# Performance work log

Measured on AMD Instinct MI355X. Metric: run time of the kernel, lower is better.

Reference implementation:

```python
import jax, jax.numpy as jnp
import numpy as np

N_NODES = 50000
N_EDGES = 800000
IN_CH = 128
HID = 64
OUT_CH = 64


def sage_conv(x, src, dst, w_l, w_r, b, num_nodes):
    """PyG SAGEConv with mean aggregation: lin_l(mean_j x_j) + lin_r(x_i)."""
    # gather source features and scatter-mean into destination nodes
    agg = jax.ops.segment_sum(x[src], dst, num_segments=num_nodes)          # [N, C]
    deg = jax.ops.segment_sum(jnp.ones((src.shape[0],), x.dtype), dst,
                              num_segments=num_nodes)                        # [N]
    mean = agg / jnp.maximum(deg, 1.0)[:, None]
    return mean @ w_l + x @ w_r + b


def setup_inputs() -> dict:
    key = jax.random.key(0)
    k = jax.random.split(key, 8)
    x = jax.random.normal(k[0], (N_NODES, IN_CH), dtype=jnp.float32)
    edge_index = jax.random.randint(k[1], (2, N_EDGES), 0, N_NODES, dtype=jnp.int32)
    s1 = 1.0 / np.sqrt(IN_CH)
    s2 = 1.0 / np.sqrt(HID)
    w1_l = jax.random.uniform(k[2], (IN_CH, HID), jnp.float32, -s1, s1)
    w1_r = jax.random.uniform(k[3], (IN_CH, HID), jnp.float32, -s1, s1)
    b1 = jax.random.uniform(k[4], (HID,), jnp.float32, -s1, s1)
    w2_l = jax.random.uniform(k[5], (HID, OUT_CH), jnp.float32, -s2, s2)
    w2_r = jax.random.uniform(k[6], (HID, OUT_CH), jnp.float32, -s2, s2)
    b2 = jax.random.uniform(k[7], (OUT_CH,), jnp.float32, -s2, s2)
    return {"x": x, "edge_index": edge_index,
            "w1_l": w1_l, "w1_r": w1_r, "b1": b1,
            "w2_l": w2_l, "w2_r": w2_r, "b2": b2}


def reference(x, edge_index, w1_l, w1_r, b1, w2_l, w2_r, b2):
    src, dst = edge_index[0], edge_index[1]
    num_nodes = x.shape[0]
    h = jax.nn.relu(sage_conv(x, src, dst, w1_l, w1_r, b1, num_nodes))
    out = jax.nn.relu(sage_conv(h, src, dst, w2_l, w2_r, b2, num_nodes))
    return out
```

## Files before the change

kernel.cpp:

```cpp
#include <hip/hip_runtime.h>
#include <hip/hip_fp16.h>

#define DEGCAP 64
#define NB_MAX 256
#define BCAP 5120
#define TILE 4000

typedef _Float16 half8 __attribute__((ext_vector_type(8)));
typedef float float4v __attribute__((ext_vector_type(4)));

__global__ __launch_bounds__(256) void prep(int* __restrict__ bCursor,
                                            const float* __restrict__ w1l,
                                            const float* __restrict__ w1r,
                                            const float* __restrict__ w2l,
                                            const float* __restrict__ w2r,
                                            _Float16* __restrict__ Wt1,
                                            _Float16* __restrict__ Wt2) {
    const int gtid = blockIdx.x * 256 + threadIdx.x;
    const int gstride = gridDim.x * 256;
    if (gtid < NB_MAX) bCursor[gtid] = 0;
    for (int i = gtid; i < 128 * 128; i += gstride) {
        int c = i >> 7, k = i & 127;
        const float* W = (c < 64) ? w1l : w1r;
        Wt1[c * 128 + k] = (_Float16)W[k * 64 + (c & 63)];
    }
    for (int i = gtid; i < 128 * 64; i += gstride) {
        int c = i >> 6, k = i & 63;
        const float* W = (c < 64) ? w2l : w2r;
        Wt2[c * 64 + k] = (_Float16)W[k * 64 + (c & 63)];
    }
}

template <int K, bool AF32>
__device__ __forceinline__ void gemm_body(const void* __restrict__ Av,
                                          const _Float16* __restrict__ Wt,
                                          unsigned short* __restrict__ Clh,
                                          unsigned short* __restrict__ Trh,
                                          int M, int blk) {
    constexpr int NS = K / 32;
    const int tid = threadIdx.x;
    const int row0 = blk * 64;
    const int wv = tid >> 6;
    const int lane = tid & 63;
    const int qd = lane >> 4;
    const int lr = lane & 15;
    const int col = wv * 16 + lr;

    half8 bl[NS], br[NS];
    #pragma unroll
    for (int s = 0; s < NS; ++s) {
        bl[s] = *(const half8*)&Wt[col * K + s * 32 + qd * 8];
        br[s] = *(const half8*)&Wt[(64 + col) * K + s * 32 + qd * 8];
    }

    half8 a[4][NS];
    #pragma unroll
    for (int i = 0; i < 4; ++i) {
        const int gr = row0 + i * 16 + lr;
        const bool ok = gr < M;
        if constexpr (AF32) {
            const float* Arow = (const float*)Av + (long long)gr * K;
            #pragma unroll
            for (int s = 0; s < NS; ++s) {
                float4 t0 = make_float4(0.f, 0.f, 0.f, 0.f);
                float4 t1 = make_float4(0.f, 0.f, 0.f, 0.f);
                if (ok) {
                    t0 = *(const float4*)&Arow[s * 32 + qd * 8];
                    t1 = *(const float4*)&Arow[s * 32 + qd * 8 + 4];
                }
                half8 h;
                h[0] = (_Float16)t0.x; h[1] = (_Float16)t0.y;
                h[2] = (_Float16)t0.z; h[3] = (_Float16)t0.w;
                h[4] = (_Float16)t1.x; h[5] = (_Float16)t1.y;
                h[6] = (_Float16)t1.z; h[7] = (_Float16)t1.w;
                a[i][s] = h;
            }
        } else {
            const _Float16* Arow = (const _Float16*)Av + (long long)gr * K;
            #pragma unroll
            for (int s = 0; s < NS; ++s) {
                a[i][s] = ok ? *(const half8*)&Arow[s * 32 + qd * 8]
                             : (half8){0, 0, 0, 0, 0, 0, 0, 0};
            }
        }
    }

    float4v accL[4], accR[4];
    #pragma unroll
    for (int i = 0; i < 4; ++i) {
        accL[i] = (float4v){0.f, 0.f, 0.f, 0.f};
        accR[i] = (float4v){0.f, 0.f, 0.f, 0.f};
    }

    #pragma unroll
    for (int i = 0; i < 4; ++i) {
        #pragma unroll
        for (int s = 0; s < NS; ++s) {
            accL[i] = __builtin_amdgcn_mfma_f32_16x16x32_f16(a[i][s], bl[s], accL[i], 0, 0, 0);
            accR[i] = __builtin_amdgcn_mfma_f32_16x16x32_f16(a[i][s], br[s], accR[i], 0, 0, 0);
        }
    }

    #pragma unroll
    for (int i = 0; i < 4; ++i) {
        #pragma unroll
        for (int rg = 0; rg < 4; ++rg) {
            int gr = row0 + i * 16 + qd * 4 + rg;
            if (gr < M) {
                Clh[(long long)gr * 64 + col] = __half_as_ushort(__float2half_rn(accL[i][rg]));
                Trh[(long long)gr * 64 + col] = __half_as_ushort(__float2half_rn(accR[i][rg]));
            }
        }
    }
}

__global__ __launch_bounds__(256) void fused_scatter_gemm1(
        const int* __restrict__ src, const int* __restrict__ dst,
        int* __restrict__ bCursor, unsigned int* __restrict__ gPacked,
        int E, int NB, int scatterBlocks,
        const float* __restrict__ A, const _Float16* __restrict__ Wt1,
        unsigned short* __restrict__ Clh, unsigned short* __restrict__ Trh,
        int M) {
    __shared__ __align__(16) char smem[22048];
    const int tid = threadIdx.x;

    if ((int)blockIdx.x < scatterBlocks) {
        unsigned int* spv = (unsigned int*)smem;
        unsigned char* sbuk = (unsigned char*)(smem + 16000);
        int* hist = (int*)(smem + 20000);
        int* cur  = (int*)(smem + 21024);

        const int t0 = blockIdx.x * TILE;
        const int len = (E - t0) < TILE ? (E - t0) : TILE;

        hist[tid] = 0;
        __syncthreads();
        for (int j = tid; j < len; j += 256) {
            int d = dst[t0 + j];
            int s = src[t0 + j];
            int b = d >> 8;
            sbuk[j] = (unsigned char)b;
            spv[j] = ((unsigned int)(d & 255) << 17) | (unsigned int)s;
            atomicAdd(&hist[b], 1);
        }
        __syncthreads();
        if (tid < NB && hist[tid] > 0)
            cur[tid] = tid * BCAP + atomicAdd(&bCursor[tid], hist[tid]);
        __syncthreads();
        for (int j = tid; j < len; j += 256) {
            int b = sbuk[j];
            int pos = atomicAdd(&cur[b], 1);
            if (pos < (b + 1) * BCAP) gPacked[pos] = spv[j];
        }
    } else {
        gemm_body<128, true>(A, Wt1, Clh, Trh, M, (int)blockIdx.x - scatterBlocks);
    }
}

__global__ __launch_bounds__(256) void bucket_build(const unsigned int* __restrict__ gPacked,
                                                    const int* __restrict__ bCursor,
                                                    int* __restrict__ deg,
                                                    unsigned short* __restrict__ ssrc,
                                                    int N) {
    __shared__ int cnt[256];
    const int tid = threadIdx.x;
    const int b = blockIdx.x;
    const int base = b * BCAP;
    int C = bCursor[b];
    if (C > BCAP) C = BCAP;

    cnt[tid] = 0;
    __syncthreads();
    for (int j = tid; j < C; j += 256) {
        unsigned int v = gPacked[base + j];
        int ln = v >> 17;
        int pos = atomicAdd(&cnt[ln], 1);
        if (pos < DEGCAP)
            ssrc[(long long)(b * 256 + ln) * DEGCAP + pos] = (unsigned short)(v & 0x1FFFFu);
    }
    __syncthreads();
    int node = b * 256 + tid;
    if (node < N) deg[node] = cnt[tid] < DEGCAP ? cnt[tid] : DEGCAP;
}

__global__ __launch_bounds__(256) void gemm2(const _Float16* __restrict__ Ah,
                                             const _Float16* __restrict__ Wt2,
                                             unsigned short* __restrict__ Clh,
                                             unsigned short* __restrict__ Trh,
                                             int M) {
    gemm_body<64, false>(Ah, Wt2, Clh, Trh, M, (int)blockIdx.x);
}

template <bool OUTH>
__global__ __launch_bounds__(256) void agg_group(const uint2* __restrict__ TL,
                                                 const uint2* __restrict__ TR,
                                                 const float* __restrict__ bias,
                                                 const int* __restrict__ deg_,
                                                 const uint2* __restrict__ ssrc2,
                                                 void* __restrict__ outv, int N) {
    const int tid = threadIdx.x;
    const int wv = tid >> 6;
    const int lane = tid & 63;
    const int c = lane & 15;
    const int w = (int)blockIdx.x * 16 + wv * 4 + (lane >> 4);
    const bool ok = w < N;

    const int deg = ok ? deg_[w] : 0;
    const int n = deg < DEGCAP ? deg : DEGCAP;

    uint2 su = ok ? ssrc2[(size_t)w * 16 + c] : make_uint2(0u, 0u);

    float a0 = 0.f, a1 = 0.f, a2 = 0.f, a3 = 0.f;

    for (int j = 0; j < n; j += 4) {
        const int b = (lane & 48) + (j >> 2);
        unsigned sx = __shfl((int)su.x, b, 64);
        unsigned sy = __shfl((int)su.y, b, 64);
        int e0 = (int)(sx & 0xFFFFu);
        int e1 = (int)(sx >> 16);
        int e2 = (int)(sy & 0xFFFFu);
        int e3 = (int)(sy >> 16);
        uint2 q0 = TL[e0 * 16 + c];
        uint2 q1 = TL[e1 * 16 + c];
        uint2 q2 = TL[e2 * 16 + c];
        uint2 q3 = TL[e3 * 16 + c];
        float2 f;
        f = __half22float2(*(__half2*)&q0.x); a0 += f.x; a1 += f.y;
        f = __half22float2(*(__half2*)&q0.y); a2 += f.x; a3 += f.y;
        if (j + 1 < n) {
            f = __half22float2(*(__half2*)&q1.x); a0 += f.x; a1 += f.y;
            f = __half22float2(*(__half2*)&q1.y); a2 += f.x; a3 += f.y;
        }
        if (j + 2 < n) {
            f = __half22float2(*(__half2*)&q2.x); a0 += f.x; a1 += f.y;
            f = __half22float2(*(__half2*)&q2.y); a2 += f.x; a3 += f.y;
        }
        if (j + 3 < n) {
            f = __half22float2(*(__half2*)&q3.x); a0 += f.x; a1 += f.y;
            f = __half22float2(*(__half2*)&q3.y); a2 += f.x; a3 += f.y;
        }
    }

    if (ok) {
        float d = (float)(deg > 1 ? deg : 1);
        uint2 tu = TR[(size_t)w * 16 + c];
        float2 t0 = __half22float2(*(__half2*)&tu.x);
        float2 t1 = __half22float2(*(__half2*)&tu.y);
        float4 bb = *(const float4*)&bias[c * 4];
        float v0 = fmaxf(a0 / d + t0.x + bb.x, 0.f);
        float v1 = fmaxf(a1 / d + t0.y + bb.y, 0.f);
        float v2 = fmaxf(a2 / d + t1.x + bb.z, 0.f);
        float v3 = fmaxf(a3 / d + t1.y + bb.w, 0.f);
        if (OUTH) {
            __half2 h0 = __floats2half2_rn(v0, v1);
            __half2 h1 = __floats2half2_rn(v2, v3);
            uint2 st;
            st.x = *(unsigned int*)&h0;
            st.y = *(unsigned int*)&h1;
            ((uint2*)outv)[(size_t)w * 16 + c] = st;
        } else {
            ((float4*)outv)[(size_t)w * 16 + c] = make_float4(v0, v1, v2, v3);
        }
    }
}

extern "C" void kernel_launch(void* const* d_in, const int* in_sizes, int n_in,
                              void* d_out, int out_size, void* d_ws, size_t ws_size,
                              hipStream_t stream) {
    const float* x   = (const float*)d_in[0];
    const int*   ei  = (const int*)d_in[1];
    const float* w1l = (const float*)d_in[2];
    const float* w1r = (const float*)d_in[3];
    const float* b1  = (const float*)d_in[4];
    const float* w2l = (const float*)d_in[5];
    const float* w2r = (const float*)d_in[6];
    const float* b2  = (const float*)d_in[7];
    float* out = (float*)d_out;

    const int N = in_sizes[0] / 128;
    const int E = in_sizes[1] / 2;
    const int* src = ei;
    const int* dst = ei + E;
    const int NB = (N + 255) >> 8;

    auto alignup = [](size_t v) { return (v + 255) & ~(size_t)255; };
    char* p = (char*)d_ws;
    int* bCursor = (int*)p;                    p += alignup(NB_MAX * sizeof(int));
    int* deg     = (int*)p;                    p += alignup((size_t)N * sizeof(int));
    unsigned int* gPacked = (unsigned int*)p;  p += alignup((size_t)NB_MAX * BCAP * sizeof(unsigned int));
    unsigned short* ssrc = (unsigned short*)p; p += alignup((size_t)N * DEGCAP * sizeof(unsigned short));
    const long long NC = (long long)N * 64;
    unsigned short* tlh = (unsigned short*)p;  p += alignup((size_t)NC * sizeof(unsigned short));
    unsigned short* trh = (unsigned short*)p;  p += alignup((size_t)NC * sizeof(unsigned short));
    unsigned short* hh  = (unsigned short*)p;  p += alignup((size_t)NC * sizeof(unsigned short));
    _Float16* Wt1 = (_Float16*)p;              p += alignup(128 * 128 * sizeof(_Float16));
    _Float16* Wt2 = (_Float16*)p;              p += alignup(128 * 64 * sizeof(_Float16));

    const int scatterBlocks = (E + TILE - 1) / TILE;
    const int gemmBlocks = (N + 63) / 64;
    const int aggBlocks = (N + 15) / 16;

    prep<<<96, 256, 0, stream>>>(bCursor, w1l, w1r, w2l, w2r, Wt1, Wt2);

    fused_scatter_gemm1<<<scatterBlocks + gemmBlocks, 256, 0, stream>>>(
        src, dst, bCursor, gPacked, E, NB, scatterBlocks,
        x, Wt1, tlh, trh, N);

    bucket_build<<<NB, 256, 0, stream>>>(gPacked, bCursor, deg, ssrc, N);

    agg_group<true><<<aggBlocks, 256, 0, stream>>>((const uint2*)tlh,
                                                   (const uint2*)trh,
                                                   b1, deg, (const uint2*)ssrc,
                                                   hh, N);

    gemm2<<<gemmBlocks, 256, 0, stream>>>((const _Float16*)hh, Wt2, tlh, trh, N);

    agg_group<false><<<aggBlocks, 256, 0, stream>>>((const uint2*)tlh,
                                                    (const uint2*)trh,
                                                    b2, deg, (const uint2*)ssrc,
                                                    out, N);
}
```

Before: 172.1 us.

## Fuse layer-1 aggregation with layer-2 GEMM via shared-memory tile

Merges the first aggregation kernel and the second-layer GEMM into one kernel. Each block aggregates 16 nodes, stages the fp16 hidden rows in LDS, then runs MFMA against Wt2 and writes the left and right projections to new ping-pong buffers. This drops one kernel launch and the global write and re-read of the hidden activation. In exchange, the weights are reloaded per 16-row block instead of per 64-row block, and the output stores are narrow 2-byte scalar writes.

```diff
diff --git a/kernel.cpp b/kernel.cpp
--- a/kernel.cpp
+++ b/kernel.cpp
@@ -31,12 +31,12 @@
     }
 }
 
-template <int K, bool AF32>
-__device__ __forceinline__ void gemm_body(const void* __restrict__ Av,
-                                          const _Float16* __restrict__ Wt,
-                                          unsigned short* __restrict__ Clh,
-                                          unsigned short* __restrict__ Trh,
-                                          int M, int blk) {
+template <int K>
+__device__ __forceinline__ void gemm_body_f32(const float* __restrict__ Av,
+                                              const _Float16* __restrict__ Wt,
+                                              unsigned short* __restrict__ Clh,
+                                              unsigned short* __restrict__ Trh,
+                                              int M, int blk) {
     constexpr int NS = K / 32;
     const int tid = threadIdx.x;
     const int row0 = blk * 64;
@@ -58,30 +58,21 @@
     for (int i = 0; i < 4; ++i) {
         const int gr = row0 + i * 16 + lr;
         const bool ok = gr < M;
-        if constexpr (AF32) {
-            const float* Arow = (const float*)Av + (long long)gr * K;
-            #pragma unroll
-            for (int s = 0; s < NS; ++s) {
-                float4 t0 = make_float4(0.f, 0.f, 0.f, 0.f);
-                float4 t1 = make_float4(0.f, 0.f, 0.f, 0.f);
-                if (ok) {
-                    t0 = *(const float4*)&Arow[s * 32 + qd * 8];
-                    t1 = *(const float4*)&Arow[s * 32 + qd * 8 + 4];
-                }
-                half8 h;
-                h[0] = (_Float16)t0.x; h[1] = (_Float16)t0.y;
-                h[2] = (_Float16)t0.z; h[3] = (_Float16)t0.w;
-                h[4] = (_Float16)t1.x; h[5] = (_Float16)t1.y;
-                h[6] = (_Float16)t1.z; h[7] = (_Float16)t1.w;
-                a[i][s] = h;
+        const float* Arow = Av + (long long)gr * K;
+        #pragma unroll
+        for (int s = 0; s < NS; ++s) {
+            float4 t0 = make_float4(0.f, 0.f, 0.f, 0.f);
+            float4 t1 = make_float4(0.f, 0.f, 0.f, 0.f);
+            if (ok) {
+                t0 = *(const float4*)&Arow[s * 32 + qd * 8];
+                t1 = *(const float4*)&Arow[s * 32 + qd * 8 + 4];
             }
-        } else {
-            const _Float16* Arow = (const _Float16*)Av + (long long)gr * K;
-            #pragma unroll
-            for (int s = 0; s < NS; ++s) {
-                a[i][s] = ok ? *(const half8*)&Arow[s * 32 + qd * 8]
-                             : (half8){0, 0, 0, 0, 0, 0, 0, 0};
-            }
+            half8 h;
+            h[0] = (_Float16)t0.x; h[1] = (_Float16)t0.y;
+            h[2] = (_Float16)t0.z; h[3] = (_Float16)t0.w;
+            h[4] = (_Float16)t1.x; h[5] = (_Float16)t1.y;
+            h[6] = (_Float16)t1.z; h[7] = (_Float16)t1.w;
+            a[i][s] = h;
         }
     }
 
@@ -153,7 +144,7 @@
             if (pos < (b + 1) * BCAP) gPacked[pos] = spv[j];
         }
     } else {
-        gemm_body<128, true>(A, Wt1, Clh, Trh, M, (int)blockIdx.x - scatterBlocks);
+        gemm_body_f32<128>(A, Wt1, Clh, Trh, M, (int)blockIdx.x - scatterBlocks);
     }
 }
 
@@ -183,35 +174,17 @@
     if (node < N) deg[node] = cnt[tid] < DEGCAP ? cnt[tid] : DEGCAP;
 }
 
-__global__ __launch_bounds__(256) void gemm2(const _Float16* __restrict__ Ah,
-                                             const _Float16* __restrict__ Wt2,
-                                             unsigned short* __restrict__ Clh,
-                                             unsigned short* __restrict__ Trh,
-                                             int M) {
-    gemm_body<64, false>(Ah, Wt2, Clh, Trh, M, (int)blockIdx.x);
-}
-
-template <bool OUTH>
-__global__ __launch_bounds__(256) void agg_group(const uint2* __restrict__ TL,
-                                                 const uint2* __restrict__ TR,
-                                                 const float* __restrict__ bias,
-                                                 const int* __restrict__ deg_,
-                                                 const uint2* __restrict__ ssrc2,
-                                                 void* __restrict__ outv, int N) {
-    const int tid = threadIdx.x;
-    const int wv = tid >> 6;
-    const int lane = tid & 63;
-    const int c = lane & 15;
-    const int w = (int)blockIdx.x * 16 + wv * 4 + (lane >> 4);
-    const bool ok = w < N;
-
+__device__ __forceinline__ float4 agg_node(const uint2* __restrict__ TL,
+                                           const uint2* __restrict__ TR,
+                                           const float* __restrict__ bias,
+                                           const int* __restrict__ deg_,
+                                           const uint2* __restrict__ ssrc2,
+                                           int w, int lane, int c, bool ok) {
     const int deg = ok ? deg_[w] : 0;
     const int n = deg < DEGCAP ? deg : DEGCAP;
-
     uint2 su = ok ? ssrc2[(size_t)w * 16 + c] : make_uint2(0u, 0u);
 
     float a0 = 0.f, a1 = 0.f, a2 = 0.f, a3 = 0.f;
-
     for (int j = 0; j < n; j += 4) {
         const int b = (lane & 48) + (j >> 2);
         unsigned sx = __shfl((int)su.x, b, 64);
@@ -241,27 +214,97 @@
         }
     }
 
+    float4 r = make_float4(0.f, 0.f, 0.f, 0.f);
     if (ok) {
         float d = (float)(deg > 1 ? deg : 1);
         uint2 tu = TR[(size_t)w * 16 + c];
         float2 t0 = __half22float2(*(__half2*)&tu.x);
         float2 t1 = __half22float2(*(__half2*)&tu.y);
         float4 bb = *(const float4*)&bias[c * 4];
-        float v0 = fmaxf(a0 / d + t0.x + bb.x, 0.f);
-        float v1 = fmaxf(a1 / d + t0.y + bb.y, 0.f);
-        float v2 = fmaxf(a2 / d + t1.x + bb.z, 0.f);
-        float v3 = fmaxf(a3 / d + t1.y + bb.w, 0.f);
-        if (OUTH) {
-            __half2 h0 = __floats2half2_rn(v0, v1);
-            __half2 h1 = __floats2half2_rn(v2, v3);
-            uint2 st;
-            st.x = *(unsigned int*)&h0;
-            st.y = *(unsigned int*)&h1;
-            ((uint2*)outv)[(size_t)w * 16 + c] = st;
-        } else {
-            ((float4*)outv)[(size_t)w * 16 + c] = make_float4(v0, v1, v2, v3);
-        }
-    }
+        r.x = fmaxf(a0 / d + t0.x + bb.x, 0.f);
+        r.y = fmaxf(a1 / d + t0.y + bb.y, 0.f);
+        r.z = fmaxf(a2 / d + t1.x + bb.z, 0.f);
+        r.w = fmaxf(a3 / d + t1.y + bb.w, 0.f);
+    }
+    return r;
+}
+
+__global__ __launch_bounds__(256) void agg1_gemm2(const uint2* __restrict__ TL,
+                                                  const uint2* __restrict__ TR,
+                                                  const float* __restrict__ b1,
+                                                  const int* __restrict__ deg_,
+                                                  const uint2* __restrict__ ssrc2,
+                                                  const _Float16* __restrict__ Wt2,
+                                                  unsigned short* __restrict__ Cl2,
+                                                  unsigned short* __restrict__ Tr2,
+                                                  int N) {
+    __shared__ _Float16 xs[16 * 72];
+    const int tid = threadIdx.x;
+    const int wv = tid >> 6;
+    const int lane = tid & 63;
+    const int c = lane & 15;
+    const int row = wv * 4 + (lane >> 4);
+    const int w = (int)blockIdx.x * 16 + row;
+    const bool ok = w < N;
+
+    float4 h = agg_node(TL, TR, b1, deg_, ssrc2, w, lane, c, ok);
+    {
+        __half2 h0 = __floats2half2_rn(h.x, h.y);
+        __half2 h1 = __floats2half2_rn(h.z, h.w);
+        uint2 st;
+        st.x = *(unsigned int*)&h0;
+        st.y = *(unsigned int*)&h1;
+        *(uint2*)&xs[row * 72 + c * 4] = st;
+    }
+    __syncthreads();
+
+    const int qd = lane >> 4;
+    const int lr = lane & 15;
+    const int col = wv * 16 + lr;
+    const int row0 = (int)blockIdx.x * 16;
+
+    half8 bl[2], br[2], a[2];
+    #pragma unroll
+    for (int s = 0; s < 2; ++s) {
+        bl[s] = *(const half8*)&Wt2[col * 64 + s * 32 + qd * 8];
+        br[s] = *(const half8*)&Wt2[(64 + col) * 64 + s * 32 + qd * 8];
+        a[s]  = *(const half8*)&xs[lr * 72 + s * 32 + qd * 8];
+    }
+
+    float4v accL = (float4v){0.f, 0.f, 0.f, 0.f};
+    float4v accR = (float4v){0.f, 0.f, 0.f, 0.f};
+    #pragma unroll
+    for (int s = 0; s < 2; ++s) {
+        accL = __builtin_amdgcn_mfma_f32_16x16x32_f16(a[s], bl[s], accL, 0, 0, 0);
+        accR = __builtin_amdgcn_mfma_f32_16x16x32_f16(a[s], br[s], accR, 0, 0, 0);
+    }
+
+    #pragma unroll
+    for (int rg = 0; rg < 4; ++rg) {
+        int gr = row0 + qd * 4 + rg;
+        if (gr < N) {
+            Cl2[(long long)gr * 64 + col] = __half_as_ushort(__float2half_rn(accL[rg]));
+            Tr2[(long long)gr * 64 + col] = __half_as_ushort(__float2half_rn(accR[rg]));
+        }
+    }
+}
+
+__global__ __launch_bounds__(256) void agg2(const uint2* __restrict__ TL,
+                                            const uint2* __restrict__ TR,
+                                            const float* __restrict__ bias,
+                                            const int* __restrict__ deg_,
+                                            const uint2* __restrict__ ssrc2,
+                                            float* __restrict__ outv, int N) {
+    const int tid = threadIdx.x;
+    const int wv = tid >> 6;
+    const int lane = tid & 63;
+    const int c = lane & 15;
+    const int w = (int)blockIdx.x * 16 + wv * 4 + (lane >> 4);
+    const bool ok = w < N;
+
+    float4 r = agg_node(TL, TR, bias, deg_, ssrc2, w, lane, c, ok);
+    if (ok)
+        ((float4*)outv)[(size_t)w * 16 + c] = r;
 }
 
 extern "C" void kernel_launch(void* const* d_in, const int* in_sizes, int n_in,
@@ -291,8 +334,9 @@
     unsigned short* ssrc = (unsigned short*)p; p += alignup((size_t)N * DEGCAP * sizeof(unsigned short));
     const long long NC = (long long)N * 64;
     unsigned short* tlh = (unsigned short*)p;  p += alignup((size_t)NC * sizeof(unsigned short));
+    unsigned short* tl2 = (unsigned short*)p;  p += alignup((size_t)NC * sizeof(unsigned short));
     unsigned short* trh = (unsigned short*)p;  p += alignup((size_t)NC * sizeof(unsigned short));
-    unsigned short* hh  = (unsigned short*)p;  p += alignup((size_t)NC * sizeof(unsigned short));
+    unsigned short* tr2 = (unsigned short*)p;  p += alignup((size_t)NC * sizeof(unsigned short));
     _Float16* Wt1 = (_Float16*)p;              p += alignup(128 * 128 * sizeof(_Float16));
     _Float16* Wt2 = (_Float16*)p;              p += alignup(128 * 64 * sizeof(_Float16));
 
@@ -308,15 +352,13 @@
 
     bucket_build<<<NB, 256, 0, stream>>>(gPacked, bCursor, deg, ssrc, N);
 
-    agg_group<true><<<aggBlocks, 256, 0, stream>>>((const uint2*)tlh,
-                                                   (const uint2*)trh,
-                                                   b1, deg, (const uint2*)ssrc,
-                                                   hh, N);
-
-    gemm2<<<gemmBlocks, 256, 0, stream>>>((const _Float16*)hh, Wt2, tlh, trh, N);
-
-    agg_group<false><<<aggBlocks, 256, 0, stream>>>((const uint2*)tlh,
-                                                    (const uint2*)trh,
-                                                    b2, deg, (const uint2*)ssrc,
-                                                    out, N);
-}
+    agg1_gemm2<<<aggBlocks, 256, 0, stream>>>((const uint2*)tlh,
+                                              (const uint2*)trh,
+                                              b1, deg, (const uint2*)ssrc,
+                                              Wt2, tl2, tr2, N);
+
+    agg2<<<aggBlocks, 256, 0, stream>>>((const uint2*)tl2,
+                                        (const uint2*)tr2,
+                                        b2, deg, (const uint2*)ssrc,
+                                        out, N);
+}
```

Result: faster. 163.6 us (-4.9%).
